# Optimization experiments

Hardware: AMD Instinct MI355X
Metric: run time of the kernel (lower is better)

Reference implementation:

```python
import jax, jax.numpy as jnp
import numpy as np

N, F, C = 4096, 512, 512
NUM_HOPS, TOP_K, MASK_RATIO = 3, 8, 0.5
EPS = 1e-12


def setup_inputs() -> dict:
    key = jax.random.key(0)
    ks = jax.random.split(key, 8)
    return {
        "x": jax.random.normal(ks[0], (N, F), dtype=jnp.float32),
        "adj": jax.random.uniform(ks[1], (NUM_HOPS, N, N), dtype=jnp.float32),
        "rand_mask": jax.random.uniform(ks[2], (NUM_HOPS, N, N), dtype=jnp.float32),
        "W_in": jax.random.normal(ks[3], (F, C), dtype=jnp.float32) * 0.02,
        "b_in": jnp.zeros((C,), dtype=jnp.float32),
        "W_out": jax.random.normal(ks[4], (C, C), dtype=jnp.float32) * 0.02,
        "b_out": jnp.zeros((C,), dtype=jnp.float32),
        "alpha": jnp.ones((NUM_HOPS,), dtype=jnp.float32),
        "beta": jnp.full((1,), 0.5, dtype=jnp.float32),
    }


def reference(x, adj, rand_mask, W_in, b_in, W_out, b_out, alpha, beta):
    H_low = x @ W_in + b_in  # (N, C)
    # F.normalize(x, dim=-1) @ F.normalize(x.T, dim=0) == x_n @ x_n.T
    xn = x / jnp.maximum(jnp.linalg.norm(x, axis=-1, keepdims=True), EPS)
    sim = xn @ xn.T  # (N, N)
    a = jax.nn.softmax(alpha)
    rows = jnp.arange(N)[:, None]
    H_high = jnp.zeros((N, F), dtype=x.dtype)
    for k in range(NUM_HOPS):
        Akw = a[k] * adj[k] * sim  # (N, N)
        _, idx = jax.lax.top_k(Akw, TOP_K)  # (N, TOP_K)
        topk_mask = jnp.zeros_like(Akw).at[rows, idx].set(1.0)
        retain = (rand_mask[k] < MASK_RATIO).astype(Akw.dtype)
        final_mask = ((topk_mask + retain) > 0).astype(Akw.dtype)
        Hk = (Akw * final_mask) @ x  # (N, F)
        H_high = H_high + a[k] * Hk
    b = beta[0]
    H = jax.nn.relu(b * H_low + (1.0 - b) * H_high)
    # dropout in eval mode (identity)
    out = H @ W_out + b_out
    return jax.nn.log_softmax(out, axis=-1)
```

## Files before the change

### kernel.cpp

```cpp
#include <hip/hip_runtime.h>
#include <hip/hip_bf16.h>
#include <stdint.h>

#define NROW 4096
#define FDIM 512

typedef short bf16x8 __attribute__((ext_vector_type(8)));
typedef float f32x4 __attribute__((ext_vector_type(4)));
typedef float f4 __attribute__((ext_vector_type(4)));
typedef ushort u16x4 __attribute__((ext_vector_type(4)));

#define NEG_INF (-__builtin_inff())

__device__ inline ushort f2bf(float f) {
    union { float f; uint32_t u; } c{f};
    uint32_t u = c.u;
    uint32_t r = (u + 0x7FFF + ((u >> 16) & 1)) >> 16;
    return (ushort)r;
}
__device__ inline uint32_t cvt_pk_bf16(float lo, float hi) {
    uint32_t r;
    asm("v_cvt_pk_bf16_f32 %0, %1, %2" : "=v"(r) : "v"(lo), "v"(hi));
    return r;
}
__device__ inline float up0(uint32_t p) {
    union { uint32_t u; float f; } c{p << 16}; return c.f;
}
__device__ inline float up1(uint32_t p) {
    union { uint32_t u; float f; } c{p & 0xFFFF0000u}; return c.f;
}

__device__ inline float waveReduceMax(float v) {
    #pragma unroll
    for (int o = 32; o > 0; o >>= 1) v = fmaxf(v, __shfl_xor(v, o));
    return v;
}
__device__ inline float waveReduceSum(float v) {
    #pragma unroll
    for (int o = 32; o > 0; o >>= 1) v += __shfl_xor(v, o);
    return v;
}

__device__ inline void CE(float& a, float& b) {
    float mx = fmaxf(a, b);
    b = fminf(a, b);
    a = mx;
}
__device__ inline void sort8(float (&l)[8]) {
    CE(l[0],l[1]); CE(l[2],l[3]); CE(l[4],l[5]); CE(l[6],l[7]);
    CE(l[0],l[2]); CE(l[1],l[3]); CE(l[4],l[6]); CE(l[5],l[7]);
    CE(l[1],l[2]); CE(l[5],l[6]);
    CE(l[0],l[4]); CE(l[1],l[5]); CE(l[2],l[6]); CE(l[3],l[7]);
    CE(l[2],l[4]); CE(l[3],l[5]);
    CE(l[1],l[2]); CE(l[3],l[4]); CE(l[5],l[6]);
}
__device__ inline void mergeTop8(float (&a)[8], const float (&b)[8]) {
    float t[8];
    #pragma unroll
    for (int i = 0; i < 8; i++) t[i] = fmaxf(a[i], b[7 - i]);
    CE(t[0],t[4]); CE(t[1],t[5]); CE(t[2],t[6]); CE(t[3],t[7]);
    CE(t[0],t[2]); CE(t[1],t[3]); CE(t[4],t[6]); CE(t[5],t[7]);
    CE(t[0],t[1]); CE(t[2],t[3]); CE(t[4],t[5]); CE(t[6],t[7]);
    #pragma unroll
    for (int i = 0; i < 8; i++) a[i] = t[i];
}

#define GLL16(src, dst)                                                        \
    __builtin_amdgcn_global_load_lds(                                          \
        (const __attribute__((address_space(1))) void*)(src),                  \
        (__attribute__((address_space(3))) void*)(dst), 16, 0, 0)

__global__ __launch_bounds__(64) void coef_k(const float* __restrict__ alpha,
                                             const float* __restrict__ beta,
                                             float* __restrict__ coef) {
    if (threadIdx.x == 0) {
        float a0 = alpha[0], a1 = alpha[1], a2 = alpha[2];
        float m = fmaxf(a0, fmaxf(a1, a2));
        float e0 = expf(a0 - m), e1 = expf(a1 - m), e2 = expf(a2 - m);
        float s = e0 + e1 + e2;
        coef[0] = e0 / s; coef[1] = e1 / s; coef[2] = e2 / s;
        coef[3] = beta[0];
    }
}

__global__ __launch_bounds__(256) void prep_fused(
    const float* __restrict__ x, ushort* __restrict__ xn,
    ushort* __restrict__ xb, ushort* __restrict__ xbT,
    const float* __restrict__ W_in, ushort* __restrict__ WinT,
    const float* __restrict__ W_out, ushort* __restrict__ WoutT) {
    const int b = blockIdx.x;
    const int tid = threadIdx.x;
    __shared__ float b4[4];
    __shared__ ushort t[64][65];

    if (b < 4096) {
        const int row = b;
        int lane = tid & 63, w = tid >> 6;
        const float* xr = x + (size_t)row * FDIM;
        float v0 = xr[tid], v1 = xr[tid + 256];
        float ss = v0 * v0 + v1 * v1;
        ss = waveReduceSum(ss);
        if (lane == 0) b4[w] = ss;
        __syncthreads();
        float tot = b4[0] + b4[1] + b4[2] + b4[3];
        float inv = 1.f / fmaxf(sqrtf(tot), 1e-12f);
        size_t o = (size_t)row * FDIM + tid;
        xn[o] = f2bf(v0 * inv);  xn[o + 256] = f2bf(v1 * inv);
        xb[o] = f2bf(v0);        xb[o + 256] = f2bf(v1);
    } else if (b < 4608) {
        const int tb = b - 4096;
        const int c0 = (tb & 7) * 64, r0 = (tb >> 3) * 64;
        int lx = tid & 63, ly = tid >> 6;
        #pragma unroll
        for (int i = 0; i < 16; i++)
            t[ly + 4 * i][lx] = f2bf(x[(size_t)(r0 + ly + 4 * i) * FDIM + c0 + lx]);
        __syncthreads();
        #pragma unroll
        for (int i = 0; i < 16; i++)
            xbT[(size_t)(c0 + ly + 4 * i) * NROW + r0 + lx] = t[lx][ly + 4 * i];
    } else {
        const int cb = b - 4608;
        const float* Wf = (cb >> 6) ? W_out : W_in;
        ushort* WT = (cb >> 6) ? WoutT : WinT;
        const int idx = cb & 63;
        const int c0 = (idx & 7) * 64, r0 = (idx >> 3) * 64;
        int lx = tid & 63, ly = tid >> 6;
        #pragma unroll
        for (int i = 0; i < 16; i++)
            t[ly + 4 * i][lx] = f2bf(Wf[(size_t)(r0 + ly + 4 * i) * 512 + c0 + lx]);
        __syncthreads();
        #pragma unroll
        for (int i = 0; i < 16; i++)
            WT[(size_t)(c0 + ly + 4 * i) * 512 + r0 + lx] = t[lx][ly + 4 * i];
    }
}

__global__ __launch_bounds__(256) void gemm_sym(
    const ushort* __restrict__ A, ushort* __restrict__ C) {
    constexpr int BK = 64;
    constexpr int NT = 128 * BK;
    __shared__ __align__(16) ushort smem[128 * 130];
    ushort* As = smem;
    ushort* Bs = smem + NT;

    int bi = 0, rem = blockIdx.x;
    while (rem >= 32 - bi) { rem -= 32 - bi; bi++; }
    const int bj = bi + rem;
    const int m0 = bi * 128, n0 = bj * 128;

    const int tid = threadIdx.x;
    const int lane = tid & 63, w = tid >> 6;
    const int wr = w >> 1, wc = w & 1;

    f32x4 acc[4][4];
    #pragma unroll
    for (int mi = 0; mi < 4; mi++)
        #pragma unroll
        for (int ni = 0; ni < 4; ni++)
            #pragma unroll
            for (int r = 0; r < 4; r++) acc[mi][ni][r] = 0.f;

    for (int k0 = 0; k0 < FDIM; k0 += BK) {
        #pragma unroll
        for (int p = 0; p < 4; ++p) {
            int chunk = p * 256 + tid;
            int row = chunk / 8;
            int kc = chunk % 8;
            GLL16(A + (size_t)(m0 + row) * FDIM + k0 + kc * 8,
                  As + (size_t)(p * 256 + w * 64) * 8);
            GLL16(A + (size_t)(n0 + row) * FDIM + k0 + kc * 8,
                  Bs + (size_t)(p * 256 + w * 64) * 8);
        }
        __syncthreads();
        #pragma unroll
        for (int kf = 0; kf < BK / 32; ++kf) {
            const int ko = kf * 32 + (lane >> 4) * 8;
            bf16x8 av[4], bv[4];
            #pragma unroll
            for (int mi = 0; mi < 4; mi++)
                av[mi] = *(const bf16x8*)&As[(wr * 64 + mi * 16 + (lane & 15)) * BK + ko];
            #pragma unroll
            for (int ni = 0; ni < 4; ni++)
                bv[ni] = *(const bf16x8*)&Bs[(wc * 64 + ni * 16 + (lane & 15)) * BK + ko];
            #pragma unroll
            for (int mi = 0; mi < 4; mi++)
                #pragma unroll
                for (int ni = 0; ni < 4; ni++)
                    acc[mi][ni] = __builtin_amdgcn_mfma_f32_16x16x32_bf16(
                        av[mi], bv[ni], acc[mi][ni], 0, 0, 0);
        }
        __syncthreads();
    }

    #pragma unroll
    for (int mi = 0; mi < 4; mi++) {
        #pragma unroll
        for (int ni = 0; ni < 4; ni++) {
            int lcol = wc * 64 + ni * 16 + (lane & 15);
            #pragma unroll
            for (int r = 0; r < 4; r++) {
                int lrow = wr * 64 + mi * 16 + (lane >> 4) * 4 + r;
                ushort hv = f2bf(acc[mi][ni][r]);
                C[(size_t)(m0 + lrow) * NROW + n0 + lcol] = hv;
                smem[lrow * 130 + lcol] = hv;
            }
        }
    }

    if (bi != bj) {
        __syncthreads();
        const int wv = w;
        #pragma unroll 4
        for (int i = 0; i < 32; i++) {
            int r2 = wv * 32 + i;
            ushort a = smem[(lane * 2) * 130 + r2];
            ushort bb = smem[(lane * 2 + 1) * 130 + r2];
            uint32_t pk = (uint32_t)a | ((uint32_t)bb << 16);
            *(uint32_t*)&C[(size_t)(n0 + r2) * NROW + m0 + lane * 2] = pk;
        }
    }
}

template <int EPI>
__global__ __launch_bounds__(256) void gemm_abT(
    const ushort* __restrict__ A, int lda,
    const ushort* __restrict__ B, int ldb,
    int Kdim, int ldc,
    float* __restrict__ Cf, ushort* __restrict__ Cb,
    const float* __restrict__ bias) {
    constexpr int BK = 64;
    constexpr int NT = 128 * BK;
    constexpr int CPR = BK / 8;
    constexpr int PASSES = (128 * CPR) / 256;
    __shared__ __align__(16) ushort smem[2 * NT];
    ushort* As = smem;
    ushort* Bs = smem + NT;

    if constexpr (EPI == 3) {
        A += (size_t)blockIdx.z * 1024;
        B += (size_t)blockIdx.z * 1024;
        Cf += (size_t)blockIdx.z * ((size_t)NROW * 512);
    }

    const int tid = threadIdx.x;
    const int lane = tid & 63, w = tid >> 6;
    const int wr = w >> 1, wc = w & 1;
    const int m0 = blockIdx.y * 128;
    const int n0 = blockIdx.x * 128;

    f32x4 acc[4][4];
    #pragma unroll
    for (int mi = 0; mi < 4; mi++)
        #pragma unroll
        for (int ni = 0; ni < 4; ni++)
            #pragma unroll
            for (int r = 0; r < 4; r++) acc[mi][ni][r] = 0.f;

    for (int k0 = 0; k0 < Kdim; k0 += BK) {
        #pragma unroll
        for (int p = 0; p < PASSES; ++p) {
            int chunk = p * 256 + tid;
            int row = chunk / CPR;
            int kc = chunk % CPR;
            const ushort* asrc = A + (size_t)(m0 + row) * lda + k0 + kc * 8;
            const ushort* bsrc = B + (size_t)(n0 + row) * ldb + k0 + kc * 8;
            ushort* abase = As + (size_t)(p * 256 + w * 64) * 8;
            ushort* bbase = Bs + (size_t)(p * 256 + w * 64) * 8;
            GLL16(asrc, abase);
            GLL16(bsrc, bbase);
        }
        __syncthreads();
        #pragma unroll
        for (int kf = 0; kf < BK / 32; ++kf) {
            const int ko = kf * 32 + (lane >> 4) * 8;
            bf16x8 av[4], bv[4];
            #pragma unroll
            for (int mi = 0; mi < 4; mi++)
                av[mi] = *(const bf16x8*)&As[(wr * 64 + mi * 16 + (lane & 15)) * BK + ko];
            #pragma unroll
            for (int ni = 0; ni < 4; ni++)
                bv[ni] = *(const bf16x8*)&Bs[(wc * 64 + ni * 16 + (lane & 15)) * BK + ko];
            #pragma unroll
            for (int mi = 0; mi < 4; mi++)
                #pragma unroll
                for (int ni = 0; ni < 4; ni++)
                    acc[mi][ni] = __builtin_amdgcn_mfma_f32_16x16x32_bf16(
                        av[mi], bv[ni], acc[mi][ni], 0, 0, 0);
        }
        __syncthreads();
    }

    #pragma unroll
    for (int mi = 0; mi < 4; mi++) {
        #pragma unroll
        for (int ni = 0; ni < 4; ni++) {
            int col = n0 + wc * 64 + ni * 16 + (lane & 15);
            #pragma unroll
            for (int r = 0; r < 4; r++) {
                int rowg = m0 + wr * 64 + mi * 16 + (lane >> 4) * 4 + r;
                size_t off = (size_t)rowg * ldc + col;
                float v = acc[mi][ni][r];
                if constexpr (EPI == 1) {
                    Cf[off] = v + bias[col];
                } else {
                    Cf[off] = v;
                }
            }
        }
    }
}

__global__ __launch_bounds__(256) void topk_build_M(
    const ushort* __restrict__ simb, const float* __restrict__ adj,
    const float* __restrict__ rmask, const float* __restrict__ coef,
    ushort* __restrict__ Mout) {
    const int tid = threadIdx.x;
    const int lane = tid & 63;
    const int w = tid >> 6;
    const int row = blockIdx.x;
    __shared__ float wl[3][4][8];

    const int cbase = w * 1024 + lane * 4;
    const size_t hopstride = (size_t)NROW * NROW;

    const ushort* srow = simb + (size_t)row * NROW + cbase;
    const float* arow = adj + (size_t)row * NROW + cbase;
    const float* rrow = rmask + (size_t)row * NROW + cbase;

    uint2 svp[4];
    #pragma unroll
    for (int q = 0; q < 4; q++)
        svp[q] = *(const uint2*)(srow + q * 256);

    float macc[4][4];
    #pragma unroll
    for (int q = 0; q < 4; q++)
        #pragma unroll
        for (int c = 0; c < 4; c++) macc[q][c] = 0.f;

    #pragma unroll 1
    for (int k = 0; k < 3; ++k) {
        const float* ar = arow + (size_t)k * hopstride;
        const float* rr = rrow + (size_t)k * hopstride;

        f4 rv[4], a[4];
        #pragma unroll
        for (int q = 0; q < 4; q++) rv[q] = *(const f4*)(rr + q * 256);
        #pragma unroll
        for (int q = 0; q < 4; q++) a[q] = *(const f4*)(ar + q * 256);

        uint32_t rbits = 0;
        #pragma unroll
        for (int q = 0; q < 4; q++) {
            rbits |= (rv[q].x < 0.5f ? 1u : 0u) << (q * 4 + 0);
            rbits |= (rv[q].y < 0.5f ? 1u : 0u) << (q * 4 + 1);
            rbits |= (rv[q].z < 0.5f ? 1u : 0u) << (q * 4 + 2);
            rbits |= (rv[q].w < 0.5f ? 1u : 0u) << (q * 4 + 3);
        }

        uint2 avp[4];
        #pragma unroll
        for (int q = 0; q < 4; q++) {
            avp[q].x = cvt_pk_bf16(a[q].x, a[q].y);
            avp[q].y = cvt_pk_bf16(a[q].z, a[q].w);
        }

        float lo8[8], hi8[8];
        #pragma unroll
        for (int qq = 0; qq < 2; qq++) {
            lo8[qq * 4 + 0] = up0(avp[qq].x) * up0(svp[qq].x);
            lo8[qq * 4 + 1] = up1(avp[qq].x) * up1(svp[qq].x);
            lo8[qq * 4 + 2] = up0(avp[qq].y) * up0(svp[qq].y);
            lo8[qq * 4 + 3] = up1(avp[qq].y) * up1(svp[qq].y);
        }
        #pragma unroll
        for (int qq = 0; qq < 2; qq++) {
            const int q = 2 + qq;
            hi8[qq * 4 + 0] = up0(avp[q].x) * up0(svp[q].x);
            hi8[qq * 4 + 1] = up1(avp[q].x) * up1(svp[q].x);
            hi8[qq * 4 + 2] = up0(avp[q].y) * up0(svp[q].y);
            hi8[qq * 4 + 3] = up1(avp[q].y) * up1(svp[q].y);
        }
        sort8(lo8);
        sort8(hi8);
        mergeTop8(lo8, hi8);

        #pragma unroll
        for (int lvl = 0; lvl < 6; lvl++) {
            float b[8];
            #pragma unroll
            for (int i = 0; i < 8; i++) b[i] = __shfl_xor(lo8[i], 1 << lvl);
            mergeTop8(lo8, b);
        }

        if (lane < 8) wl[k][w][lane] = lo8[lane];
        __syncthreads();
        #pragma unroll
        for (int ww = 0; ww < 4; ww++) {
            if (ww != w) {
                float b[8];
                #pragma unroll
                for (int i = 0; i < 8; i++) b[i] = wl[k][ww][i];
                mergeTop8(lo8, b);
            }
        }
        const float thr = lo8[7];

        const float ak = coef[k];
        const float aksq = ak * ak;
        #pragma unroll
        for (int q = 0; q < 4; q++) {
            float av0 = up0(avp[q].x), av1 = up1(avp[q].x);
            float av2 = up0(avp[q].y), av3 = up1(avp[q].y);
            float s0 = up0(svp[q].x), s1 = up1(svp[q].x);
            float s2 = up0(svp[q].y), s3 = up1(svp[q].y);
            bool m0 = ((rbits >> (q * 4 + 0)) & 1) || (av0 * s0 >= thr);
            bool m1 = ((rbits >> (q * 4 + 1)) & 1) || (av1 * s1 >= thr);
            bool m2 = ((rbits >> (q * 4 + 2)) & 1) || (av2 * s2 >= thr);
            bool m3 = ((rbits >> (q * 4 + 3)) & 1) || (av3 * s3 >= thr);
            macc[q][0] += m0 ? aksq * av0 : 0.f;
            macc[q][1] += m1 ? aksq * av1 : 0.f;
            macc[q][2] += m2 ? aksq * av2 : 0.f;
            macc[q][3] += m3 ? aksq * av3 : 0.f;
        }
        __syncthreads();
    }

    ushort* mrow = Mout + (size_t)row * NROW + cbase;
    #pragma unroll
    for (int q = 0; q < 4; q++) {
        u16x4 o;
        o[0] = f2bf(up0(svp[q].x) * macc[q][0]);
        o[1] = f2bf(up1(svp[q].x) * macc[q][1]);
        o[2] = f2bf(up0(svp[q].y) * macc[q][2]);
        o[3] = f2bf(up1(svp[q].y) * macc[q][3]);
        *(u16x4*)(mrow + q * 256) = o;
    }
}

__global__ __launch_bounds__(256) void reduce_relu(
    const float* __restrict__ parts, const float* __restrict__ hlow,
    const float* __restrict__ coef, ushort* __restrict__ Hb) {
    const size_t i = (size_t)blockIdx.x * 256 + threadIdx.x;
    const f4* p4 = (const f4*)parts;
    f4 s = p4[i];
    #pragma unroll
    for (int z = 1; z < 4; z++) s += p4[(size_t)z * 524288 + i];
    f4 hl = ((const f4*)hlow)[i];
    float cb = coef[3];
    u16x4 o;
    #pragma unroll
    for (int c = 0; c < 4; c++) {
        float h = cb * hl[c] + (1.f - cb) * s[c];
        o[c] = f2bf(fmaxf(h, 0.f));
    }
    *((u16x4*)Hb + i) = o;
}

__global__ __launch_bounds__(256) void logsoftmax_k(const float* __restrict__ L,
                                                    float* __restrict__ out) {
    int row = blockIdx.x, tid = threadIdx.x;
    int lane = tid & 63, w = tid >> 6;
    const float* lr = L + (size_t)row * 512;
    float v0 = lr[tid], v1 = lr[tid + 256];
    __shared__ float bm[4], bs[4];
    float m = fmaxf(v0, v1);
    m = waveReduceMax(m);
    if (lane == 0) bm[w] = m;
    __syncthreads();
    float M = fmaxf(fmaxf(bm[0], bm[1]), fmaxf(bm[2], bm[3]));
    float s = expf(v0 - M) + expf(v1 - M);
    s = waveReduceSum(s);
    if (lane == 0) bs[w] = s;
    __syncthreads();
    float S = bs[0] + bs[1] + bs[2] + bs[3];
    float lse = M + logf(S);
    float* orow = out + (size_t)row * 512;
    orow[tid] = v0 - lse;
    orow[tid + 256] = v1 - lse;
}

extern "C" void kernel_launch(void* const* d_in, const int* in_sizes, int n_in,
                              void* d_out, int out_size, void* d_ws, size_t ws_size,
                              hipStream_t stream) {
    const float* x     = (const float*)d_in[0];
    const float* adj   = (const float*)d_in[1];
    const float* rmask = (const float*)d_in[2];
    const float* W_in  = (const float*)d_in[3];
    const float* b_in  = (const float*)d_in[4];
    const float* W_out = (const float*)d_in[5];
    const float* b_out = (const float*)d_in[6];
    const float* alpha = (const float*)d_in[7];
    const float* beta  = (const float*)d_in[8];
    float* out = (float*)d_out;

    const size_t MB = 1024 * 1024;
    char* wsb = (char*)d_ws;
    ushort* simb   = (ushort*)wsb;
    float*  parts  = (float*)wsb;
    float*  logits = (float*)wsb;
    ushort* Mb     = (ushort*)(wsb + 32 * MB);
    ushort* xn     = (ushort*)(wsb + 64 * MB);
    ushort* xb     = (ushort*)(wsb + 68 * MB);
    ushort* xbT    = (ushort*)(wsb + 72 * MB);
    ushort* WinT   = (ushort*)(wsb + 76 * MB);
    ushort* WoutT  = (ushort*)(wsb + 76 * MB + 512 * 1024);
    float*  Hlow   = (float*)(wsb + 77 * MB);
    ushort* Hb     = (ushort*)(wsb + 85 * MB);
    float*  coef   = (float*)(wsb + 89 * MB);

    coef_k<<<1, 64, 0, stream>>>(alpha, beta, coef);

    prep_fused<<<4096 + 512 + 128, 256, 0, stream>>>(
        x, xn, xb, xbT, W_in, WinT, W_out, WoutT);

    gemm_sym<<<528, 256, 0, stream>>>(xn, simb);

    topk_build_M<<<NROW, 256, 0, stream>>>(simb, adj, rmask, coef, Mb);

    gemm_abT<1><<<dim3(4, 32), 256, 0, stream>>>(
        xb, FDIM, WinT, FDIM, FDIM, 512, Hlow, nullptr, b_in);

    gemm_abT<3><<<dim3(4, 32, 4), 256, 0, stream>>>(
        Mb, NROW, xbT, NROW, 1024, 512, parts, nullptr, nullptr);

    reduce_relu<<<2048, 256, 0, stream>>>(parts, Hlow, coef, Hb);

    gemm_abT<1><<<dim3(4, 32), 256, 0, stream>>>(
        Hb, 512, WoutT, 512, 512, 512, logits, nullptr, b_out);

    logsoftmax_k<<<NROW, 256, 0, stream>>>(logits, out);
}
```

Before: 213.5 us.

## Fuse H_low GEMM into split-K GEMM launch and process two rows per top-k block

Folds the x@W_in GEMM into the split-K M@x launch as a fifth z-slice, with bias added later in reduce_relu, which removes one kernel launch and lets the small GEMM share the grid. The top-k kernel now handles two rows per 512-thread block. The final cross-wave merge computes only the 8th-largest threshold through a cheaper min/max network instead of a full merge. Together these cut launch overhead and tail effects, at the cost of heavier blocks and a z-slice whose K-length (512) differs from the others (1024), so work per block is uneven.

```diff
diff --git a/kernel.cpp b/kernel.cpp
--- a/kernel.cpp
+++ b/kernel.cpp
@@ -63,6 +63,13 @@
     CE(t[0],t[1]); CE(t[2],t[3]); CE(t[4],t[5]); CE(t[6],t[7]);
     #pragma unroll
     for (int i = 0; i < 8; i++) a[i] = t[i];
+}
+__device__ inline float merge8th(const float (&a)[8], const float (&b)[8]) {
+    float t0 = fminf(fmaxf(a[0], b[7]), fmaxf(a[1], b[6]));
+    float t1 = fminf(fmaxf(a[2], b[5]), fmaxf(a[3], b[4]));
+    float t2 = fminf(fmaxf(a[4], b[3]), fmaxf(a[5], b[2]));
+    float t3 = fminf(fmaxf(a[6], b[1]), fmaxf(a[7], b[0]));
+    return fminf(fminf(t0, t1), fminf(t2, t3));
 }
 
 #define GLL16(src, dst)                                                        \
@@ -227,7 +234,9 @@
     const ushort* __restrict__ B, int ldb,
     int Kdim, int ldc,
     float* __restrict__ Cf, ushort* __restrict__ Cb,
-    const float* __restrict__ bias) {
+    const float* __restrict__ bias,
+    const ushort* __restrict__ A2, const ushort* __restrict__ B2,
+    float* __restrict__ Cf4) {
     constexpr int BK = 64;
     constexpr int NT = 128 * BK;
     constexpr int CPR = BK / 8;
@@ -236,10 +245,16 @@
     ushort* As = smem;
     ushort* Bs = smem + NT;
 
+    int Kd = Kdim;
     if constexpr (EPI == 3) {
-        A += (size_t)blockIdx.z * 1024;
-        B += (size_t)blockIdx.z * 1024;
-        Cf += (size_t)blockIdx.z * ((size_t)NROW * 512);
+        if (blockIdx.z == 4) {
+            A = A2; lda = FDIM; B = B2; ldb = FDIM; Kd = FDIM;
+            Cf = Cf4;
+        } else {
+            A += (size_t)blockIdx.z * 1024;
+            B += (size_t)blockIdx.z * 1024;
+            Cf += (size_t)blockIdx.z * ((size_t)NROW * 512);
+        }
     }
 
     const int tid = threadIdx.x;
@@ -256,7 +271,7 @@
             #pragma unroll
             for (int r = 0; r < 4; r++) acc[mi][ni][r] = 0.f;
 
-    for (int k0 = 0; k0 < Kdim; k0 += BK) {
+    for (int k0 = 0; k0 < Kd; k0 += BK) {
         #pragma unroll
         for (int p = 0; p < PASSES; ++p) {
             int chunk = p * 256 + tid;
@@ -310,17 +325,19 @@
     }
 }
 
-__global__ __launch_bounds__(256) void topk_build_M(
+__global__ __launch_bounds__(512) void topk_build_M(
     const ushort* __restrict__ simb, const float* __restrict__ adj,
     const float* __restrict__ rmask, const float* __restrict__ coef,
     ushort* __restrict__ Mout) {
     const int tid = threadIdx.x;
     const int lane = tid & 63;
     const int w = tid >> 6;
-    const int row = blockIdx.x;
-    __shared__ float wl[3][4][8];
-
-    const int cbase = w * 1024 + lane * 4;
+    const int rloc = w >> 2;
+    const int wv = w & 3;
+    const int row = blockIdx.x * 2 + rloc;
+    __shared__ float wl[2][3][4][8];
+
+    const int cbase = wv * 1024 + lane * 4;
     const size_t hopstride = (size_t)NROW * NROW;
 
     const ushort* srow = simb + (size_t)row * NROW + cbase;
@@ -393,18 +410,19 @@
             mergeTop8(lo8, b);
         }
 
-        if (lane < 8) wl[k][w][lane] = lo8[lane];
-        __syncthreads();
-        #pragma unroll
-        for (int ww = 0; ww < 4; ww++) {
-            if (ww != w) {
-                float b[8];
-                #pragma unroll
-                for (int i = 0; i < 8; i++) b[i] = wl[k][ww][i];
-                mergeTop8(lo8, b);
-            }
-        }
-        const float thr = lo8[7];
+        if (lane < 8) wl[rloc][k][wv][lane] = lo8[lane];
+        __syncthreads();
+        float b0[8], b1[8], b2[8];
+        const int o0 = (wv + 1) & 3, o1 = (wv + 2) & 3, o2 = (wv + 3) & 3;
+        #pragma unroll
+        for (int i = 0; i < 8; i++) b0[i] = wl[rloc][k][o0][i];
+        #pragma unroll
+        for (int i = 0; i < 8; i++) b1[i] = wl[rloc][k][o1][i];
+        #pragma unroll
+        for (int i = 0; i < 8; i++) b2[i] = wl[rloc][k][o2][i];
+        mergeTop8(lo8, b0);
+        mergeTop8(lo8, b1);
+        const float thr = merge8th(lo8, b2);
 
         const float ak = coef[k];
         const float aksq = ak * ak;
@@ -439,14 +457,15 @@
 }
 
 __global__ __launch_bounds__(256) void reduce_relu(
-    const float* __restrict__ parts, const float* __restrict__ hlow,
-    const float* __restrict__ coef, ushort* __restrict__ Hb) {
+    const float* __restrict__ parts, const float* __restrict__ parts4,
+    const float* __restrict__ bias, const float* __restrict__ coef,
+    ushort* __restrict__ Hb) {
     const size_t i = (size_t)blockIdx.x * 256 + threadIdx.x;
     const f4* p4 = (const f4*)parts;
     f4 s = p4[i];
     #pragma unroll
     for (int z = 1; z < 4; z++) s += p4[(size_t)z * 524288 + i];
-    f4 hl = ((const f4*)hlow)[i];
+    f4 hl = ((const f4*)parts4)[i] + ((const f4*)bias)[i & 127];
     float cb = coef[3];
     u16x4 o;
     #pragma unroll
@@ -505,7 +524,7 @@
     ushort* xbT    = (ushort*)(wsb + 72 * MB);
     ushort* WinT   = (ushort*)(wsb + 76 * MB);
     ushort* WoutT  = (ushort*)(wsb + 76 * MB + 512 * 1024);
-    float*  Hlow   = (float*)(wsb + 77 * MB);
+    float*  parts4 = (float*)(wsb + 77 * MB);
     ushort* Hb     = (ushort*)(wsb + 85 * MB);
     float*  coef   = (float*)(wsb + 89 * MB);
 
@@ -516,18 +535,17 @@
 
     gemm_sym<<<528, 256, 0, stream>>>(xn, simb);
 
-    topk_build_M<<<NROW, 256, 0, stream>>>(simb, adj, rmask, coef, Mb);
+    topk_build_M<<<NROW / 2, 512, 0, stream>>>(simb, adj, rmask, coef, Mb);
+
+    gemm_abT<3><<<dim3(4, 32, 5), 256, 0, stream>>>(
+        Mb, NROW, xbT, NROW, 1024, 512, parts, nullptr, nullptr,
+        xb, WinT, parts4);
+
+    reduce_relu<<<2048, 256, 0, stream>>>(parts, parts4, b_in, coef, Hb);
 
     gemm_abT<1><<<dim3(4, 32), 256, 0, stream>>>(
-        xb, FDIM, WinT, FDIM, FDIM, 512, Hlow, nullptr, b_in);
-
-    gemm_abT<3><<<dim3(4, 32, 4), 256, 0, stream>>>(
-        Mb, NROW, xbT, NROW, 1024, 512, parts, nullptr, nullptr);
-
-    reduce_relu<<<2048, 256, 0, stream>>>(parts, Hlow, coef, Hb);
-
-    gemm_abT<1><<<dim3(4, 32), 256, 0, stream>>>(
-        Hb, 512, WoutT, 512, 512, 512, logits, nullptr, b_out);
+        Hb, 512, WoutT, 512, 512, 512, logits, nullptr, b_out,
+        nullptr, nullptr, nullptr);
 
     logsoftmax_k<<<NROW, 256, 0, stream>>>(logits, out);
 }
```

After: 210.0 us. Within noise of the previous version (-1.6%).
